# Performance work log

Measured on AMD Instinct MI355X. Metric: run time of the kernel, lower is better.

## Reference

```python
import jax, jax.numpy as jnp
import numpy as np

B = 32768      # number of graphs in the batch
NPG = 54       # nodes per graph (fixed by reshape(batch_size, 54*4))
EPG = 144      # directed edges per graph (Catan board: 72 undirected)
N = B * NPG
E = B * EPG
GLOB = 10


def _lin(k, fan_in, fan_out):
    lim = 1.0 / np.sqrt(fan_in)
    kw, kb = jax.random.split(k)
    W = jax.random.uniform(kw, (fan_in, fan_out), jnp.float32, -lim, lim)
    b = jax.random.uniform(kb, (fan_out,), jnp.float32, -lim, lim)
    return W, b


def setup_inputs() -> dict:
    key = jax.random.key(0)
    ks = jax.random.split(key, 16)
    x = jax.random.normal(ks[0], (N, 8), jnp.float32)
    # PyG-style batched edge_index: edges stay within each 54-node block
    base = (jnp.arange(B, dtype=jnp.int32) * NPG)[:, None]
    src = (jax.random.randint(ks[1], (B, EPG), 0, NPG, jnp.int32) + base).reshape(-1)
    dst = (jax.random.randint(ks[2], (B, EPG), 0, NPG, jnp.int32) + base).reshape(-1)
    edge_index = jnp.stack([src, dst], axis=0)
    edge_attr = jax.random.uniform(ks[3], (E,), jnp.float32)
    globalFeats = jax.random.normal(ks[4], (B, GLOB), jnp.float32)
    # GraphConv 1: in=8 -> hidden=16  (lin_rel has bias, lin_root has no bias)
    W_rel1, b1 = _lin(ks[5], 8, 16)
    W_root1, _ = _lin(ks[6], 8, 16)
    # GraphConv 2: 16 -> 4
    W_rel2, b2 = _lin(ks[7], 16, 4)
    W_root2, _ = _lin(ks[8], 16, 4)
    # Global MLP: 10 -> 8 -> 8 -> 10
    Wg1, bg1 = _lin(ks[9], GLOB, 8)
    Wg2, bg2 = _lin(ks[10], 8, 8)
    Wg3, bg3 = _lin(ks[11], 8, GLOB)
    # Out MLP: 54*4 + 10 = 226 -> 128 -> 1
    Wo1, bo1 = _lin(ks[12], NPG * 4 + GLOB, 128)
    Wo2, bo2 = _lin(ks[13], 128, 1)
    return dict(x=x, edge_index=edge_index, edge_attr=edge_attr,
                globalFeats=globalFeats,
                W_rel1=W_rel1, b1=b1, W_root1=W_root1,
                W_rel2=W_rel2, b2=b2, W_root2=W_root2,
                Wg1=Wg1, bg1=bg1, Wg2=Wg2, bg2=bg2, Wg3=Wg3, bg3=bg3,
                Wo1=Wo1, bo1=bo1, Wo2=Wo2, bo2=bo2, isTrain=0)


def _graph_conv(x, src, dst, edge_attr, W_rel, b, W_root):
    # PyG GraphConv (aggr='add'): out = lin_rel(sum_j w_ij * x_j) + lin_root(x)
    msg = edge_attr[:, None] * x[src]                       # [E, F_in]
    agg = jax.ops.segment_sum(msg, dst, num_segments=N)     # [N, F_in]
    return agg @ W_rel + b + x @ W_root


def reference(x, edge_index, edge_attr, globalFeats,
              W_rel1, b1, W_root1, W_rel2, b2, W_root2,
              Wg1, bg1, Wg2, bg2, Wg3, bg3, Wo1, bo1, Wo2, bo2, isTrain):
    src, dst = edge_index[0], edge_index[1]
    h = jax.nn.relu(_graph_conv(x, src, dst, edge_attr, W_rel1, b1, W_root1))
    h = jax.nn.relu(_graph_conv(h, src, dst, edge_attr, W_rel2, b2, W_root2))
    embeds = h.reshape(B, NPG * 4)                          # [B, 216]
    g = jax.nn.relu(globalFeats @ Wg1 + bg1)
    g = jax.nn.relu(g @ Wg2 + bg2)
    g = jax.nn.relu(g @ Wg3 + bg3)
    out = jnp.concatenate([embeds, g], axis=-1)             # [B, 226]
    # dropout p=0.2 with isTrain=0 (eval) -> identity
    out = jax.nn.relu(out @ Wo1 + bo1)
    out = jax.nn.sigmoid(out @ Wo2 + bo2)                   # [B, 1]
    return out
```

## Files before the change

kernel.cpp:

```cpp
#include <hip/hip_runtime.h>
#include <hip/hip_fp16.h>
#include <math.h>

#define NPG 54
#define EPG 144
#define GLOB 10
#define KPAD 256
#define GPB 2

typedef _Float16 f16x8 __attribute__((ext_vector_type(8)));
typedef _Float16 f16x4 __attribute__((ext_vector_type(4)));
typedef float    f32x4 __attribute__((ext_vector_type(4)));

#define WSYNC() asm volatile("s_waitcnt lgkmcnt(0)" ::: "memory")

struct __align__(16) GL {
    _Float16 Adj[64][72];
    _Float16 XH[16][72];
};

__global__ __launch_bounds__(128, 4) void graph_kernel(
    const float* __restrict__ x,
    const int*   __restrict__ edge_index,
    const float* __restrict__ edge_attr,
    const float* __restrict__ W_rel1, const float* __restrict__ b1,
    const float* __restrict__ W_root1,
    const float* __restrict__ W_rel2, const float* __restrict__ b2,
    const float* __restrict__ W_root2,
    _Float16* __restrict__ v_out,
    int E_total)
{
    __shared__ GL S[GPB];
    const int tid  = threadIdx.x;
    const int w    = tid >> 6;
    const int lane = tid & 63;
    const int ln15 = lane & 15;
    const int quad = lane >> 4;
    const int g    = blockIdx.x * GPB + w;
    GL& L = S[w];
    const int nbase = g * NPG;
    const int ebase = g * EPG;

    _Float16 (*cat)[40] = (_Float16(*)[40])&L.Adj[0][0];

    int   esrc_r[3], edst_r[3];
    float ea_r[3];
    #pragma unroll
    for (int k = 0; k < 3; k++) {
        int e = lane + 64 * k;
        if (e < EPG) {
            esrc_r[k] = edge_index[ebase + e] - nbase;
            edst_r[k] = edge_index[(size_t)E_total + ebase + e] - nbase;
            ea_r[k]   = edge_attr[ebase + e];
        } else { esrc_r[k] = 0; edst_r[k] = -1; ea_r[k] = 0.0f; }
    }
    f16x8 xv = {0, 0, 0, 0, 0, 0, 0, 0};
    if (lane < NPG) {
        const float4* xg4 = (const float4*)(x + (size_t)(nbase + lane) * 8);
        float4 lo = xg4[0], hi = xg4[1];
        xv = (f16x8){ (_Float16)lo.x, (_Float16)lo.y, (_Float16)lo.z, (_Float16)lo.w,
                      (_Float16)hi.x, (_Float16)hi.y, (_Float16)hi.z, (_Float16)hi.w };
    }

    f16x8 wf1 = {0, 0, 0, 0, 0, 0, 0, 0};
    if (quad == 0) {
        #pragma unroll
        for (int j = 0; j < 8; j++) wf1[j] = (_Float16)W_rel1[j * 16 + ln15];
    } else if (quad == 1) {
        #pragma unroll
        for (int j = 0; j < 8; j++) wf1[j] = (_Float16)W_root1[j * 16 + ln15];
    }
    f16x8 wf2 = {0, 0, 0, 0, 0, 0, 0, 0};
    if (ln15 < 4) {
        #pragma unroll
        for (int j = 0; j < 8; j++) {
            int k = quad * 8 + j;
            wf2[j] = (_Float16)((k < 16) ? W_rel2[k * 4 + ln15]
                                         : W_root2[(k - 16) * 4 + ln15]);
        }
    }
    const float b1v = b1[ln15];
    const float b2v = b2[ln15 & 3];

    {
        uint4* z = (uint4*)&L;
        #pragma unroll
        for (int i = lane; i < 720; i += 64) z[i] = make_uint4(0, 0, 0, 0);
    }
    if (lane < NPG) {
        #pragma unroll
        for (int f = 0; f < 8; f++) L.XH[f][lane] = xv[f];
    }
    WSYNC();

    #pragma unroll
    for (int k = 0; k < 3; k++) {
        if (edst_r[k] >= 0) {
            int s = esrc_r[k];
            __half2* cell = (__half2*)&L.Adj[edst_r[k]][s & ~1];
            __half a16 = __float2half(ea_r[k]);
            __half z16 = __float2half(0.0f);
            __half2 val = (s & 1) ? __halves2half2(z16, a16)
                                  : __halves2half2(a16, z16);
            unsafeAtomicAdd(cell, val);
        }
    }
    WSYNC();

    f16x8 af[4][2];
    #pragma unroll
    for (int t = 0; t < 4; t++)
        #pragma unroll
        for (int ks = 0; ks < 2; ks++)
            af[t][ks] = *(const f16x8*)&L.Adj[t * 16 + ln15][ks * 32 + quad * 8];
    WSYNC();

    if (lane < NPG) *(f16x8*)&cat[lane][8] = xv;
    *(f16x8*)&cat[lane][16] = (f16x8){0, 0, 0, 0, 0, 0, 0, 0};
    *(f16x8*)&cat[lane][24] = (f16x8){0, 0, 0, 0, 0, 0, 0, 0};

    f32x4 acc1[4];
    #pragma unroll
    for (int t = 0; t < 4; t++) acc1[t] = (f32x4){0.f, 0.f, 0.f, 0.f};
    #pragma unroll
    for (int ks = 0; ks < 2; ks++) {
        f16x8 bx = *(const f16x8*)&L.XH[ln15][ks * 32 + quad * 8];
        #pragma unroll
        for (int t = 0; t < 4; t++)
            acc1[t] = __builtin_amdgcn_mfma_f32_16x16x32_f16(af[t][ks], bx, acc1[t], 0, 0, 0);
    }
    #pragma unroll
    for (int t = 0; t < 4; t++)
        #pragma unroll
        for (int r = 0; r < 4; r++)
            if (ln15 < 8) cat[t * 16 + quad * 4 + r][ln15] = (_Float16)acc1[t][r];
    WSYNC();

    f32x4 accL[4];
    #pragma unroll
    for (int t = 0; t < 4; t++) {
        f16x8 al = *(const f16x8*)&cat[t * 16 + ln15][quad * 8];
        f32x4 ci = (f32x4){b1v, b1v, b1v, b1v};
        accL[t] = __builtin_amdgcn_mfma_f32_16x16x32_f16(al, wf1, ci, 0, 0, 0);
    }
    #pragma unroll
    for (int t = 0; t < 4; t++) {
        f16x4 hp;
        #pragma unroll
        for (int r = 0; r < 4; r++) {
            int node = t * 16 + quad * 4 + r;
            float h = (node < NPG) ? fmaxf(accL[t][r], 0.0f) : 0.0f;
            hp[r] = (_Float16)h;
            cat[node][16 + ln15] = (_Float16)h;
        }
        *(f16x4*)&L.XH[ln15][t * 16 + quad * 4] = hp;
    }
    WSYNC();

    f32x4 acc2[4];
    #pragma unroll
    for (int t = 0; t < 4; t++) acc2[t] = (f32x4){0.f, 0.f, 0.f, 0.f};
    #pragma unroll
    for (int ks = 0; ks < 2; ks++) {
        f16x8 bh = *(const f16x8*)&L.XH[ln15][ks * 32 + quad * 8];
        #pragma unroll
        for (int t = 0; t < 4; t++)
            acc2[t] = __builtin_amdgcn_mfma_f32_16x16x32_f16(af[t][ks], bh, acc2[t], 0, 0, 0);
    }
    #pragma unroll
    for (int t = 0; t < 4; t++)
        #pragma unroll
        for (int r = 0; r < 4; r++)
            cat[t * 16 + quad * 4 + r][ln15] = (_Float16)acc2[t][r];
    WSYNC();

    _Float16* vt = &L.XH[0][0];
    #pragma unroll
    for (int t = 0; t < 4; t++) {
        f16x8 a2 = *(const f16x8*)&cat[t * 16 + ln15][quad * 8];
        f32x4 ci = (f32x4){b2v, b2v, b2v, b2v};
        f32x4 h2 = __builtin_amdgcn_mfma_f32_16x16x32_f16(a2, wf2, ci, 0, 0, 0);
        #pragma unroll
        for (int r = 0; r < 4; r++) {
            int node = t * 16 + quad * 4 + r;
            if (ln15 < 4 && node < NPG)
                vt[node * 4 + ln15] = (_Float16)fmaxf(h2[r], 0.0f);
        }
    }
    WSYNC();

    if (lane < 27)
        *(f16x8*)(v_out + (size_t)g * KPAD + lane * 8) = *(const f16x8*)&vt[lane * 8];
}

__global__ __launch_bounds__(256) void g_kernel(
    const float* __restrict__ gf,
    const float* __restrict__ Wg1, const float* __restrict__ bg1,
    const float* __restrict__ Wg2, const float* __restrict__ bg2,
    const float* __restrict__ Wg3, const float* __restrict__ bg3,
    _Float16* __restrict__ v_out)
{
    int row = blockIdx.x * 256 + threadIdx.x;
    const float* gr = gf + (size_t)row * GLOB;
    float t0[GLOB];
    #pragma unroll
    for (int i = 0; i < GLOB; i++) t0[i] = gr[i];
    float t1[8];
    #pragma unroll
    for (int j = 0; j < 8; j++) {
        float a = bg1[j];
        #pragma unroll
        for (int i = 0; i < GLOB; i++) a += t0[i] * Wg1[i * 8 + j];
        t1[j] = fmaxf(a, 0.0f);
    }
    float t2[8];
    #pragma unroll
    for (int j = 0; j < 8; j++) {
        float a = bg2[j];
        #pragma unroll
        for (int i = 0; i < 8; i++) a += t1[i] * Wg2[i * 8 + j];
        t2[j] = fmaxf(a, 0.0f);
    }
    float t3[GLOB];
    #pragma unroll
    for (int j = 0; j < GLOB; j++) {
        float a = bg3[j];
        #pragma unroll
        for (int i = 0; i < 8; i++) a += t2[i] * Wg3[i * GLOB + j];
        t3[j] = fmaxf(a, 0.0f);
    }
    _Float16* vr = v_out + (size_t)row * KPAD + 216;
    f16x8 v0 = { (_Float16)t3[0], (_Float16)t3[1], (_Float16)t3[2], (_Float16)t3[3],
                 (_Float16)t3[4], (_Float16)t3[5], (_Float16)t3[6], (_Float16)t3[7] };
    f16x8 v1 = { (_Float16)t3[8], (_Float16)t3[9], 0, 0, 0, 0, 0, 0 };
    f16x8 zz = { 0, 0, 0, 0, 0, 0, 0, 0 };
    *(f16x8*)(vr +  0) = v0;
    *(f16x8*)(vr +  8) = v1;
    *(f16x8*)(vr + 16) = zz;
    *(f16x8*)(vr + 24) = zz;
    *(f16x8*)(vr + 32) = zz;
}

#define BTS 264

__global__ __launch_bounds__(512) void out_mlp_mfma(
    const _Float16* __restrict__ V,
    const float* __restrict__ Wo1,
    const float* __restrict__ bo1,
    const float* __restrict__ Wo2,
    const float* __restrict__ bo2,
    float* __restrict__ out)
{
    extern __shared__ _Float16 Bt[];

    const int tid  = threadIdx.x;
    const int w    = tid >> 6;
    const int lane = tid & 63;
    const int ln15 = lane & 15;
    const int quad = lane >> 4;
    const int row0 = blockIdx.x * 128;

    float bo1v[8], wo2v[8];
    #pragma unroll
    for (int t = 0; t < 8; t++) {
        bo1v[t] = bo1[t * 16 + ln15];
        wo2v[t] = Wo2[t * 16 + ln15];
    }
    const float bo2v = bo2[0];

    const _Float16* Arow = V + (size_t)(row0 + w * 16 + ln15) * KPAD;
    f16x8 af[8];
    #pragma unroll
    for (int s = 0; s < 8; s++)
        af[s] = *(const f16x8*)(Arow + s * 32 + quad * 8);

    {
        int4* bz = (int4*)Bt;
        for (int i = tid; i < 4224; i += 512)
            bz[i] = make_int4(0, 0, 0, 0);
    }
    __syncthreads();
    for (int i = tid; i < 7232; i += 512) {
        int k  = i >> 5;
        int nq = (i & 31) * 4;
        float4 v = *(const float4*)(Wo1 + (size_t)k * 128 + nq);
        Bt[(nq + 0) * BTS + k] = (_Float16)v.x;
        Bt[(nq + 1) * BTS + k] = (_Float16)v.y;
        Bt[(nq + 2) * BTS + k] = (_Float16)v.z;
        Bt[(nq + 3) * BTS + k] = (_Float16)v.w;
    }
    __syncthreads();

    f32x4 acc[8];
    #pragma unroll
    for (int t = 0; t < 8; t++) acc[t] = (f32x4){0.f, 0.f, 0.f, 0.f};

    for (int s = 0; s < 8; s++) {
        #pragma unroll
        for (int t = 0; t < 8; t++) {
            f16x8 bf = *(const f16x8*)&Bt[(t * 16 + ln15) * BTS + s * 32 + quad * 8];
            acc[t] = __builtin_amdgcn_mfma_f32_16x16x32_f16(af[s], bf, acc[t], 0, 0, 0);
        }
    }

    #pragma unroll
    for (int rr = 0; rr < 4; rr++) {
        float p = 0.0f;
        #pragma unroll
        for (int t = 0; t < 8; t++) {
            float h = fmaxf(acc[t][rr] + bo1v[t], 0.0f);
            p += h * wo2v[t];
        }
        p += __shfl_xor(p, 1);
        p += __shfl_xor(p, 2);
        p += __shfl_xor(p, 4);
        p += __shfl_xor(p, 8);
        if (ln15 == rr) {
            int row = row0 + w * 16 + quad * 4 + rr;
            out[row] = 1.0f / (1.0f + expf(-(p + bo2v)));
        }
    }
}

extern "C" void kernel_launch(void* const* d_in, const int* in_sizes, int n_in,
                              void* d_out, int out_size, void* d_ws, size_t ws_size,
                              hipStream_t stream) {
    const float* x        = (const float*)d_in[0];
    const int*   ei       = (const int*)  d_in[1];
    const float* ea       = (const float*)d_in[2];
    const float* gf       = (const float*)d_in[3];
    const float* W_rel1   = (const float*)d_in[4];
    const float* b1       = (const float*)d_in[5];
    const float* W_root1  = (const float*)d_in[6];
    const float* W_rel2   = (const float*)d_in[7];
    const float* b2       = (const float*)d_in[8];
    const float* W_root2  = (const float*)d_in[9];
    const float* Wg1      = (const float*)d_in[10];
    const float* bg1      = (const float*)d_in[11];
    const float* Wg2      = (const float*)d_in[12];
    const float* bg2      = (const float*)d_in[13];
    const float* Wg3      = (const float*)d_in[14];
    const float* bg3      = (const float*)d_in[15];
    const float* Wo1      = (const float*)d_in[16];
    const float* bo1      = (const float*)d_in[17];
    const float* Wo2      = (const float*)d_in[18];
    const float* bo2      = (const float*)d_in[19];

    float* out   = (float*)d_out;
    _Float16* V  = (_Float16*)d_ws;

    const int B = out_size;
    const int E = in_sizes[1] / 2;

    graph_kernel<<<B / GPB, 128, 0, stream>>>(
        x, ei, ea,
        W_rel1, b1, W_root1, W_rel2, b2, W_root2,
        V, E);

    g_kernel<<<B / 256, 256, 0, stream>>>(gf, Wg1, bg1, Wg2, bg2, Wg3, bg3, V);

    out_mlp_mfma<<<B / 128, 512, 128 * BTS * sizeof(_Float16), stream>>>(
        V, Wo1, bo1, Wo2, bo2, out);
}
```

Measured before the change: 229.2 us.

## Fuse global MLP into output MLP and pack intermediate rows to 216 halves

```diff
diff --git a/kernel.cpp b/kernel.cpp
--- a/kernel.cpp
+++ b/kernel.cpp
@@ -5,7 +5,7 @@
 #define NPG 54
 #define EPG 144
 #define GLOB 10
-#define KPAD 256
+#define VROW 216
 #define GPB 2
 
 typedef _Float16 f16x8 __attribute__((ext_vector_type(8)));
@@ -15,7 +15,7 @@
 #define WSYNC() asm volatile("s_waitcnt lgkmcnt(0)" ::: "memory")
 
 struct __align__(16) GL {
-    _Float16 Adj[64][72];
+    _Float16 Adj[NPG][72];
     _Float16 XH[16][72];
 };
 
@@ -85,7 +85,7 @@
     {
         uint4* z = (uint4*)&L;
         #pragma unroll
-        for (int i = lane; i < 720; i += 64) z[i] = make_uint4(0, 0, 0, 0);
+        for (int i = lane; i < 630; i += 64) z[i] = make_uint4(0, 0, 0, 0);
     }
     if (lane < NPG) {
         #pragma unroll
@@ -116,8 +116,6 @@
     WSYNC();
 
     if (lane < NPG) *(f16x8*)&cat[lane][8] = xv;
-    *(f16x8*)&cat[lane][16] = (f16x8){0, 0, 0, 0, 0, 0, 0, 0};
-    *(f16x8*)&cat[lane][24] = (f16x8){0, 0, 0, 0, 0, 0, 0, 0};
 
     f32x4 acc1[4];
     #pragma unroll
@@ -190,61 +188,17 @@
     WSYNC();
 
     if (lane < 27)
-        *(f16x8*)(v_out + (size_t)g * KPAD + lane * 8) = *(const f16x8*)&vt[lane * 8];
+        *(f16x8*)(v_out + (size_t)g * VROW + lane * 8) = *(const f16x8*)&vt[lane * 8];
 }
 
-__global__ __launch_bounds__(256) void g_kernel(
+#define BTS 264
+
+__global__ __launch_bounds__(512) void out_mlp_mfma(
+    const _Float16* __restrict__ V,
     const float* __restrict__ gf,
     const float* __restrict__ Wg1, const float* __restrict__ bg1,
     const float* __restrict__ Wg2, const float* __restrict__ bg2,
     const float* __restrict__ Wg3, const float* __restrict__ bg3,
-    _Float16* __restrict__ v_out)
-{
-    int row = blockIdx.x * 256 + threadIdx.x;
-    const float* gr = gf + (size_t)row * GLOB;
-    float t0[GLOB];
-    #pragma unroll
-    for (int i = 0; i < GLOB; i++) t0[i] = gr[i];
-    float t1[8];
-    #pragma unroll
-    for (int j = 0; j < 8; j++) {
-        float a = bg1[j];
-        #pragma unroll
-        for (int i = 0; i < GLOB; i++) a += t0[i] * Wg1[i * 8 + j];
-        t1[j] = fmaxf(a, 0.0f);
-    }
-    float t2[8];
-    #pragma unroll
-    for (int j = 0; j < 8; j++) {
-        float a = bg2[j];
-        #pragma unroll
-        for (int i = 0; i < 8; i++) a += t1[i] * Wg2[i * 8 + j];
-        t2[j] = fmaxf(a, 0.0f);
-    }
-    float t3[GLOB];
-    #pragma unroll
-    for (int j = 0; j < GLOB; j++) {
-        float a = bg3[j];
-        #pragma unroll
-        for (int i = 0; i < 8; i++) a += t2[i] * Wg3[i * GLOB + j];
-        t3[j] = fmaxf(a, 0.0f);
-    }
-    _Float16* vr = v_out + (size_t)row * KPAD + 216;
-    f16x8 v0 = { (_Float16)t3[0], (_Float16)t3[1], (_Float16)t3[2], (_Float16)t3[3],
-                 (_Float16)t3[4], (_Float16)t3[5], (_Float16)t3[6], (_Float16)t3[7] };
-    f16x8 v1 = { (_Float16)t3[8], (_Float16)t3[9], 0, 0, 0, 0, 0, 0 };
-    f16x8 zz = { 0, 0, 0, 0, 0, 0, 0, 0 };
-    *(f16x8*)(vr +  0) = v0;
-    *(f16x8*)(vr +  8) = v1;
-    *(f16x8*)(vr + 16) = zz;
-    *(f16x8*)(vr + 24) = zz;
-    *(f16x8*)(vr + 32) = zz;
-}
-
-#define BTS 264
-
-__global__ __launch_bounds__(512) void out_mlp_mfma(
-    const _Float16* __restrict__ V,
     const float* __restrict__ Wo1,
     const float* __restrict__ bo1,
     const float* __restrict__ Wo2,
@@ -259,6 +213,7 @@
     const int ln15 = lane & 15;
     const int quad = lane >> 4;
     const int row0 = blockIdx.x * 128;
+    const int row  = row0 + w * 16 + ln15;
 
     float bo1v[8], wo2v[8];
     #pragma unroll
@@ -268,11 +223,49 @@
     }
     const float bo2v = bo2[0];
 
-    const _Float16* Arow = V + (size_t)(row0 + w * 16 + ln15) * KPAD;
+    float t3[GLOB];
+    {
+        const float* gr = gf + (size_t)row * GLOB;
+        float t0[GLOB];
+        #pragma unroll
+        for (int i = 0; i < GLOB; i++) t0[i] = gr[i];
+        float t1[8];
+        #pragma unroll
+        for (int j = 0; j < 8; j++) {
+            float a = bg1[j];
+            #pragma unroll
+            for (int i = 0; i < GLOB; i++) a += t0[i] * Wg1[i * 8 + j];
+            t1[j] = fmaxf(a, 0.0f);
+        }
+        float t2[8];
+        #pragma unroll
+        for (int j = 0; j < 8; j++) {
+            float a = bg2[j];
+            #pragma unroll
+            for (int i = 0; i < 8; i++) a += t1[i] * Wg2[i * 8 + j];
+            t2[j] = fmaxf(a, 0.0f);
+        }
+        #pragma unroll
+        for (int j = 0; j < GLOB; j++) {
+            float a = bg3[j];
+            #pragma unroll
+            for (int i = 0; i < 8; i++) a += t2[i] * Wg3[i * GLOB + j];
+            t3[j] = fmaxf(a, 0.0f);
+        }
+    }
+
+    const _Float16* Arow = V + (size_t)row * VROW;
     f16x8 af[8];
     #pragma unroll
-    for (int s = 0; s < 8; s++)
+    for (int s = 0; s < 6; s++)
         af[s] = *(const f16x8*)(Arow + s * 32 + quad * 8);
+    if (quad == 3)
+        af[6] = (f16x8){ (_Float16)t3[0], (_Float16)t3[1], (_Float16)t3[2], (_Float16)t3[3],
+                         (_Float16)t3[4], (_Float16)t3[5], (_Float16)t3[6], (_Float16)t3[7] };
+    else
+        af[6] = *(const f16x8*)(Arow + 192 + quad * 8);
+    af[7] = (f16x8){0, 0, 0, 0, 0, 0, 0, 0};
+    if (quad == 0) { af[7][0] = (_Float16)t3[8]; af[7][1] = (_Float16)t3[9]; }
 
     {
         int4* bz = (int4*)Bt;
@@ -316,8 +309,8 @@
         p += __shfl_xor(p, 4);
         p += __shfl_xor(p, 8);
         if (ln15 == rr) {
-            int row = row0 + w * 16 + quad * 4 + rr;
-            out[row] = 1.0f / (1.0f + expf(-(p + bo2v)));
+            int orow = row0 + w * 16 + quad * 4 + rr;
+            out[orow] = 1.0f / (1.0f + expf(-(p + bo2v)));
         }
     }
 }
@@ -357,8 +350,6 @@
         W_rel1, b1, W_root1, W_rel2, b2, W_root2,
         V, E);
 
-    g_kernel<<<B / 256, 256, 0, stream>>>(gf, Wg1, bg1, Wg2, bg2, Wg3, bg3, V);
-
     out_mlp_mfma<<<B / 128, 512, 128 * BTS * sizeof(_Float16), stream>>>(
-        V, Wo1, bo1, Wo2, bo2, out);
+        V, gf, Wg1, bg1, Wg2, bg2, Wg3, bg3, Wo1, bo1, Wo2, bo2, out);
 }
```

Measured after the change: 219.7 us. 4.1% less time.
